# Performance work log

Hardware: AMD Instinct MI355X
Metric: run time of the kernel (lower is better)

## Reference

```python
import jax, jax.numpy as jnp
import numpy as np

B, S, IN = 16, 512, 32
D, H, L = 768, 12, 6
DH = D // H
DFF = 4 * D
EPS = 1e-5
NEG = -1e9


def _ln(x, g, b):
    m = jnp.mean(x, axis=-1, keepdims=True)
    v = jnp.mean(jnp.square(x - m), axis=-1, keepdims=True)
    return (x - m) * jax.lax.rsqrt(v + EPS) * g + b


def setup_inputs() -> dict:
    key = jax.random.key(0)
    ks = jax.random.split(key, 24)
    nrm = lambda k, shape, s=0.02: jax.random.normal(k, shape, jnp.float32) * s
    inp = {
        'x': jax.random.normal(ks[0], (B, S, IN), jnp.float32),
        'event_lengths': jax.random.randint(ks[1], (B,), 1, S + 1),
        'in_w': nrm(ks[2], (IN, D)),
        'in_b': jnp.zeros((D,), jnp.float32),
        'pos_emb': nrm(ks[3], (S, D)),
        'qw': nrm(ks[4], (L, D, D)), 'qb': jnp.zeros((L, D), jnp.float32),
        'kw': nrm(ks[5], (L, D, D)), 'kb': jnp.zeros((L, D), jnp.float32),
        'vw': nrm(ks[6], (L, D, D)), 'vb': jnp.zeros((L, D), jnp.float32),
        'w1': nrm(ks[7], (L, D, DFF)), 'b1': jnp.zeros((L, DFF), jnp.float32),
        'w2': nrm(ks[8], (L, DFF, D)), 'b2': jnp.zeros((L, D), jnp.float32),
        'ln1_g': jnp.ones((L, D), jnp.float32), 'ln1_b': jnp.zeros((L, D), jnp.float32),
        'ln2_g': jnp.ones((L, D), jnp.float32), 'ln2_b': jnp.zeros((L, D), jnp.float32),
        'out_w': nrm(ks[9], (D, 1)), 'out_b': jnp.zeros((1,), jnp.float32),
    }
    return inp


def reference(x, event_lengths, in_w, in_b, pos_emb, qw, qb, kw, kb, vw, vb,
              w1, b1, w2, b2, ln1_g, ln1_b, ln2_g, ln2_b, out_w, out_b):
    b, s, _ = x.shape
    h = x @ in_w + in_b + pos_emb[None, :s]  # [B,S,D]
    valid = jnp.arange(s)[None, :] < event_lengths[:, None]  # [B,S]
    amask = valid[:, None, :, None] & valid[:, None, None, :]  # [B,1,S,S]
    scale = np.float32(1.0 / np.sqrt(DH))
    for l in range(qw.shape[0]):
        q = (h @ qw[l] + qb[l]).reshape(b, s, H, DH)
        k = (h @ kw[l] + kb[l]).reshape(b, s, H, DH)
        v = (h @ vw[l] + vb[l]).reshape(b, s, H, DH)
        scores = jnp.einsum('bqhd,bkhd->bhqk', q, k) * scale
        scores = jnp.where(amask, scores, NEG)
        p = jax.nn.softmax(scores, axis=-1)
        o = jnp.einsum('bhqk,bkhd->bqhd', p, v).reshape(b, s, -1)
        # NOTE: source overwrites summarize(...) output with the raw concat, so no out-proj
        h = _ln(h + o, ln1_g[l], ln1_b[l])
        ff = jnp.maximum(h @ w1[l] + b1[l], 0.0) @ w2[l] + b2[l]
        h = _ln(h + ff, ln2_g[l], ln2_b[l])
    pooled = jnp.where(valid[..., None], h, 0.0).sum(axis=1) / event_lengths[:, None].astype(h.dtype)
    return pooled @ out_w + out_b  # [B,1]
```

## Files before the change

### kernel.cpp

```cpp
#include <hip/hip_runtime.h>

typedef unsigned short u16;
typedef unsigned int u32;
typedef u16 u16x8 __attribute__((ext_vector_type(8)));
typedef u16 u16x4 __attribute__((ext_vector_type(4)));
typedef __bf16 bf16x8 __attribute__((ext_vector_type(8)));
typedef float f32x4 __attribute__((ext_vector_type(4)));

#define DEV __device__ __forceinline__

DEV u16 f2bf(float f) {
  u32 u = __builtin_bit_cast(u32, f);
  u32 r = u + 0x7fffu + ((u >> 16) & 1u);
  return (u16)(r >> 16);
}

DEV float bf2f(u16 v) { return __builtin_bit_cast(float, (u32)v << 16); }

DEV int imin(int a, int b) { return a < b ? a : b; }

DEV void gload_lds16(const void* g, void* l) {
  __builtin_amdgcn_global_load_lds(
      (const __attribute__((address_space(1))) void*)g,
      (__attribute__((address_space(3))) void*)l, 16, 0, 0);
}

template <int RELU, int VMODE>
__global__ __launch_bounds__(256, 3) void gemm97_kernel(
    const u16* __restrict__ A, const u16* __restrict__ Bt, const float* __restrict__ bias,
    u16* __restrict__ Cb, u16* __restrict__ vT, const int* __restrict__ lens, int M, int N, int K,
    int ldc) {
  __shared__ __align__(16) u16 As[128 * 64];
  __shared__ __align__(16) u16 Bs[128 * 64];
  const int t = threadIdx.x, wave = t >> 6, lane = t & 63;
  const int fr = lane & 15, fq = lane >> 4;
  const int NT = K >> 6;
  const int nbx = N >> 7;

  int bid = blockIdx.x;
  {
    const int cpx = (int)gridDim.x >> 3;
    bid = (bid & 7) * cpx + (bid >> 3);
  }
  const int bx = bid % nbx, by = bid / nbx;
  const int m0 = by << 7, n0 = bx << 7;
  if ((m0 & 511) >= lens[m0 >> 9]) return;

  const int srow = t >> 3;
  const int c8 = ((t & 7) ^ (srow & 7)) * 8;
  const u16* ag = A + (size_t)(m0 + srow) * K + c8;
  const u16* bg = Bt + (size_t)(n0 + srow) * K + c8;
  char* asb = (char*)As + wave * 1024;
  char* bsb = (char*)Bs + wave * 1024;

  const int wr = (wave >> 1) * 64, wc = (wave & 1) * 64;
  f32x4 acc[4][4] = {};

  for (int k0 = 0; k0 < NT; ++k0) {
#pragma unroll
    for (int i = 0; i < 4; ++i) {
      gload_lds16(ag + (size_t)i * 32 * K, asb + i * 4096);
      gload_lds16(bg + (size_t)i * 32 * K, bsb + i * 4096);
    }
    ag += 64;
    bg += 64;
    asm volatile("s_waitcnt vmcnt(0)" ::: "memory");
    __syncthreads();
#pragma unroll
    for (int ks = 0; ks < 2; ++ks) {
      bf16x8 af[4], bv[4];
#pragma unroll
      for (int m = 0; m < 4; ++m)
        af[m] = *(const bf16x8*)(As + (wr + m * 16 + fr) * 64 + (((ks * 4 + fq) ^ (fr & 7)) * 8));
#pragma unroll
      for (int n = 0; n < 4; ++n)
        bv[n] = *(const bf16x8*)(Bs + (wc + n * 16 + fr) * 64 + (((ks * 4 + fq) ^ (fr & 7)) * 8));
#pragma unroll
      for (int m = 0; m < 4; ++m)
#pragma unroll
        for (int n = 0; n < 4; ++n)
          acc[m][n] = __builtin_amdgcn_mfma_f32_16x16x32_bf16(af[m], bv[n], acc[m][n], 0, 0, 0);
    }
    __syncthreads();
  }

#pragma unroll
  for (int n = 0; n < 4; ++n) {
    const int colb = n0 + wc + n * 16;
    const int col = colb + fr;
    const float bvv = bias[col];
    if (VMODE && colb >= 1536) {
      const int dd = col - 1536;
      const int hh = dd >> 6, d6 = dd & 63;
#pragma unroll
      for (int m = 0; m < 4; ++m) {
        const int row0 = m0 + wr + m * 16 + fq * 4;
        const int bb = row0 >> 9, ss = row0 & 511;
        u16x4 pk;
#pragma unroll
        for (int r = 0; r < 4; ++r) pk[r] = f2bf(acc[m][n][r] + bvv);
        *(u16x4*)(vT + ((size_t)(bb * 12 + hh) * 64 + d6) * 512 + ss) = pk;
      }
    } else {
#pragma unroll
      for (int m = 0; m < 4; ++m) {
#pragma unroll
        for (int r = 0; r < 4; ++r) {
          const int row = m0 + wr + m * 16 + fq * 4 + r;
          float v = acc[m][n][r] + bvv;
          if (RELU) v = fmaxf(v, 0.f);
          Cb[(size_t)row * ldc + col] = f2bf(v);
        }
      }
    }
  }
}

__global__ __launch_bounds__(256) void attn_kernel(const u16* __restrict__ qk,
                                                   const u16* __restrict__ vT,
                                                   const int* __restrict__ lens,
                                                   u16* __restrict__ o) {
  __shared__ __align__(16) u16 Kl[128 * 64];
  __shared__ __align__(16) u16 Vt[64 * 128];
  __shared__ __align__(16) u16 Pl[4][16 * 128];

  const int bid = blockIdx.x;
  const int z = bid & 1;
  const int pair = bid >> 1;
  const int h = pair % 12;
  const int b = pair / 12;
  const int len = lens[b];
  if (z * 256 >= len) return;
  const int t = threadIdx.x, wave = t >> 6, lane = t & 63;
  const int fr = lane & 15, fq = lane >> 4;

  const size_t base = (size_t)b * 512 * 1536;
  const size_t vbase = (size_t)(b * 12 + h) * 64 * 512;
  const int q0w = z * 256 + wave * 64;

  bf16x8 qf[4][2];
#pragma unroll
  for (int qi = 0; qi < 4; ++qi)
#pragma unroll
    for (int ks = 0; ks < 2; ++ks)
      qf[qi][ks] = *(const bf16x8*)(qk + base + (size_t)(q0w + qi * 16 + fr) * 1536 + h * 64 +
                                    ks * 32 + fq * 8);

  f32x4 oacc[4][4] = {};
  float mrow[4][4], lrow[4][4];
#pragma unroll
  for (int qi = 0; qi < 4; ++qi)
#pragma unroll
    for (int r = 0; r < 4; ++r) {
      mrow[qi][r] = -1e30f;
      lrow[qi][r] = 0.f;
    }

  const int nt = (len + 127) >> 7;
  for (int kt = 0; kt < nt; ++kt) {
    const int kv0 = kt * 128;
#pragma unroll
    for (int i = 0; i < 4; ++i) {
      const int c = i * 256 + t;
      const int krow = c >> 3, kch = c & 7;
      u16x8 kvl = *(const u16x8*)(qk + base + (size_t)(kv0 + krow) * 1536 + 768 + h * 64 + kch * 8);
      *(u16x8*)(Kl + krow * 64 + ((kch ^ (krow & 7)) * 8)) = kvl;
      const int d = c >> 4, vch = c & 15;
      u16x8 vv = *(const u16x8*)(vT + vbase + (size_t)d * 512 + kv0 + vch * 8);
      *(u16x8*)(Vt + d * 128 + ((vch ^ (d & 7)) * 8)) = vv;
    }
    __syncthreads();

#pragma unroll
    for (int qi = 0; qi < 4; ++qi) {
      if (q0w + qi * 16 >= len) break;
      f32x4 sa[8] = {};
#pragma unroll
      for (int ks = 0; ks < 2; ++ks) {
#pragma unroll
        for (int n = 0; n < 8; ++n) {
          const int colr = n * 16 + fr;
          bf16x8 kf = *(const bf16x8*)(Kl + colr * 64 + (((ks * 4 + fq) ^ (colr & 7)) * 8));
          sa[n] = __builtin_amdgcn_mfma_f32_16x16x32_bf16(qf[qi][ks], kf, sa[n], 0, 0, 0);
        }
      }

      float tm[4] = {-1e30f, -1e30f, -1e30f, -1e30f};
#pragma unroll
      for (int n = 0; n < 8; ++n) {
        const int col = kv0 + n * 16 + fr;
        const bool ok = col < len;
#pragma unroll
        for (int r = 0; r < 4; ++r) {
          const float s = ok ? sa[n][r] * 0.125f : -1e30f;
          sa[n][r] = s;
          tm[r] = fmaxf(tm[r], s);
        }
      }
#pragma unroll
      for (int d = 1; d < 16; d <<= 1)
#pragma unroll
        for (int r = 0; r < 4; ++r) tm[r] = fmaxf(tm[r], __shfl_xor(tm[r], d));

      float al[4], rs[4];
#pragma unroll
      for (int r = 0; r < 4; ++r) {
        const float mn = fmaxf(mrow[qi][r], tm[r]);
        al[r] = __expf(mrow[qi][r] - mn);
        mrow[qi][r] = mn;
        rs[r] = 0.f;
      }
#pragma unroll
      for (int n = 0; n < 8; ++n)
#pragma unroll
        for (int r = 0; r < 4; ++r) {
          const float p = __expf(sa[n][r] - mrow[qi][r]);
          sa[n][r] = p;
          rs[r] += p;
        }
#pragma unroll
      for (int d = 1; d < 16; d <<= 1)
#pragma unroll
        for (int r = 0; r < 4; ++r) rs[r] += __shfl_xor(rs[r], d);
#pragma unroll
      for (int r = 0; r < 4; ++r) lrow[qi][r] = lrow[qi][r] * al[r] + rs[r];
#pragma unroll
      for (int n = 0; n < 4; ++n)
#pragma unroll
        for (int r = 0; r < 4; ++r) oacc[qi][n][r] *= al[r];

      u16* P = &Pl[wave][0];
#pragma unroll
      for (int n = 0; n < 8; ++n) {
        const int col = n * 16 + fr;
#pragma unroll
        for (int r = 0; r < 4; ++r) {
          const int row = fq * 4 + r;
          P[row * 128 + (((col >> 3) ^ (row & 7)) * 8) + (col & 7)] = f2bf(sa[n][r]);
        }
      }
#pragma unroll
      for (int kslot = 0; kslot < 4; ++kslot) {
        const int ch = kslot * 4 + fq;
        bf16x8 pa = *(const bf16x8*)(P + fr * 128 + ((ch ^ (fr & 7)) * 8));
#pragma unroll
        for (int n = 0; n < 4; ++n) {
          const int colv = n * 16 + fr;
          bf16x8 vf = *(const bf16x8*)(Vt + colv * 128 + ((ch ^ (colv & 7)) * 8));
          oacc[qi][n] = __builtin_amdgcn_mfma_f32_16x16x32_bf16(pa, vf, oacc[qi][n], 0, 0, 0);
        }
      }
    }
    __syncthreads();
  }

  const size_t obase = (size_t)b * 512 * 768 + (size_t)q0w * 768 + h * 64;
#pragma unroll
  for (int qi = 0; qi < 4; ++qi) {
    if (q0w + qi * 16 >= len) break;
#pragma unroll
    for (int n = 0; n < 4; ++n)
#pragma unroll
      for (int r = 0; r < 4; ++r)
        o[obase + (size_t)(qi * 16 + fq * 4 + r) * 768 + n * 16 + fr] =
            f2bf(oacc[qi][n][r] / lrow[qi][r]);
  }
}

__global__ __launch_bounds__(256) void transpose_all_kernel(
    const float* __restrict__ qw, const float* __restrict__ kw, const float* __restrict__ vw,
    const float* __restrict__ w1, const float* __restrict__ w2, u16* __restrict__ qkvt6,
    u16* __restrict__ w1t6, u16* __restrict__ w2t6) {
  __shared__ float tile[64][65];
  const int l = blockIdx.y;
  int x = blockIdx.x;
  const float* in;
  u16* op;
  int K, N, nbx;
  if (x < 432) {
    const int which = x / 144;
    x -= which * 144;
    in = (which == 0 ? qw : which == 1 ? kw : vw) + (size_t)l * 768 * 768;
    op = qkvt6 + (size_t)l * 2304 * 768 + (size_t)which * 768 * 768;
    K = 768;
    N = 768;
    nbx = 12;
  } else if (x < 1008) {
    x -= 432;
    in = w1 + (size_t)l * 768 * 3072;
    op = w1t6 + (size_t)l * 3072 * 768;
    K = 768;
    N = 3072;
    nbx = 48;
  } else {
    x -= 1008;
    in = w2 + (size_t)l * 3072 * 768;
    op = w2t6 + (size_t)l * 768 * 3072;
    K = 3072;
    N = 768;
    nbx = 12;
  }
  const int tx = threadIdx.x & 63, ty = threadIdx.x >> 6;
  const int n0 = (x % nbx) * 64, k0 = (x / nbx) * 64;
#pragma unroll
  for (int i = 0; i < 16; ++i)
    tile[ty + i * 4][tx] = in[(size_t)(k0 + ty + i * 4) * N + n0 + tx];
  __syncthreads();
#pragma unroll
  for (int i = 0; i < 16; ++i)
    op[(size_t)(n0 + ty + i * 4) * K + k0 + tx] = f2bf(tile[tx][ty + i * 4]);
}

__global__ __launch_bounds__(256) void inproj_kernel(const float* __restrict__ x,
                                                     const float* __restrict__ in_w,
                                                     const float* __restrict__ in_b,
                                                     const float* __restrict__ pos,
                                                     float* __restrict__ h,
                                                     u16* __restrict__ hbf) {
  __shared__ float xs[8][32];
  const int t = threadIdx.x;
  const int row0 = blockIdx.x * 8;
  xs[t >> 5][t & 31] = x[(size_t)row0 * 32 + t];
  __syncthreads();
#pragma unroll
  for (int j = 0; j < 3; ++j) {
    const int d = t + j * 256;
    float acc[8] = {};
#pragma unroll
    for (int i = 0; i < 32; ++i) {
      const float wv = in_w[i * 768 + d];
#pragma unroll
      for (int r = 0; r < 8; ++r) acc[r] += xs[r][i] * wv;
    }
    const float bb = in_b[d];
#pragma unroll
    for (int r = 0; r < 8; ++r) {
      const int row = row0 + r;
      const int s = row & 511;
      const float v = acc[r] + bb + pos[(size_t)s * 768 + d];
      h[(size_t)row * 768 + d] = v;
      hbf[(size_t)row * 768 + d] = f2bf(v);
    }
  }
}

__global__ __launch_bounds__(256) void ln_kernel(const float* __restrict__ hin,
                                                 const u16* __restrict__ delta,
                                                 const int* __restrict__ lens,
                                                 const float* __restrict__ g,
                                                 const float* __restrict__ bb,
                                                 float* __restrict__ hout,
                                                 u16* __restrict__ hbf) {
  const int row = blockIdx.x * 4 + (threadIdx.x >> 6);
  if ((row & 511) >= lens[row >> 9]) return;
  const int lane = threadIdx.x & 63;
  const size_t rb = (size_t)row * 768 + lane * 4;
  f32x4 xv[3];
  float s = 0.f, s2 = 0.f;
#pragma unroll
  for (int j = 0; j < 3; ++j) {
    f32x4 a = *(const f32x4*)(hin + rb + j * 256);
    u16x4 dv = *(const u16x4*)(delta + rb + j * 256);
    f32x4 v;
#pragma unroll
    for (int c = 0; c < 4; ++c) v[c] = a[c] + bf2f(dv[c]);
    xv[j] = v;
    s += v[0] + v[1] + v[2] + v[3];
    s2 += v[0] * v[0] + v[1] * v[1] + v[2] * v[2] + v[3] * v[3];
  }
#pragma unroll
  for (int d = 1; d < 64; d <<= 1) {
    s += __shfl_xor(s, d);
    s2 += __shfl_xor(s2, d);
  }
  const float mean = s * (1.f / 768.f);
  const float var = fmaxf(s2 * (1.f / 768.f) - mean * mean, 0.f);
  const float rstd = rsqrtf(var + 1e-5f);
#pragma unroll
  for (int j = 0; j < 3; ++j) {
    f32x4 gv = *(const f32x4*)(g + lane * 4 + j * 256);
    f32x4 bv = *(const f32x4*)(bb + lane * 4 + j * 256);
    f32x4 y;
    u16x4 yb;
#pragma unroll
    for (int c = 0; c < 4; ++c) {
      y[c] = (xv[j][c] - mean) * rstd * gv[c] + bv[c];
      yb[c] = f2bf(y[c]);
    }
    *(f32x4*)(hout + rb + j * 256) = y;
    *(u16x4*)(hbf + rb + j * 256) = yb;
  }
}

__global__ __launch_bounds__(256) void pool1_kernel(const float* __restrict__ h,
                                                    const int* __restrict__ lens,
                                                    const float* __restrict__ ow,
                                                    float* __restrict__ wsp) {
  const int b = blockIdx.x >> 3, chunk = blockIdx.x & 7;
  const int len = lens[b];
  const int t = threadIdx.x;
  const int s0 = chunk * 64;
  const int s1 = imin(s0 + 64, len);
  float acc0 = 0.f, acc1 = 0.f, acc2 = 0.f;
  const float* hp = h + (size_t)b * 512 * 768;
  for (int s = s0; s < s1; ++s) {
    const size_t rb = (size_t)s * 768;
    acc0 += hp[rb + t];
    acc1 += hp[rb + t + 256];
    acc2 += hp[rb + t + 512];
  }
  float part = acc0 * ow[t] + acc1 * ow[t + 256] + acc2 * ow[t + 512];
#pragma unroll
  for (int d = 1; d < 64; d <<= 1) part += __shfl_xor(part, d);
  __shared__ float ps[4];
  if ((t & 63) == 0) ps[t >> 6] = part;
  __syncthreads();
  if (t == 0) wsp[blockIdx.x] = ps[0] + ps[1] + ps[2] + ps[3];
}

__global__ void pool2_kernel(const float* __restrict__ wsp, const int* __restrict__ lens,
                             const float* __restrict__ ob, float* __restrict__ out) {
  const int b = threadIdx.x;
  if (b < 16) {
    float s = 0.f;
#pragma unroll
    for (int c = 0; c < 8; ++c) s += wsp[b * 8 + c];
    out[b] = s / (float)lens[b] + ob[0];
  }
}

__global__ void biaspack_kernel(const float* __restrict__ qb, const float* __restrict__ kb,
                                const float* __restrict__ vb, float* __restrict__ qkvb) {
  const int i = blockIdx.x * 256 + threadIdx.x;
  if (i >= 6 * 2304) return;
  const int l = i / 2304, j = i % 2304;
  float v;
  if (j < 768)
    v = qb[l * 768 + j];
  else if (j < 1536)
    v = kb[l * 768 + j - 768];
  else
    v = vb[l * 768 + j - 1536];
  qkvb[i] = v;
}

extern "C" void kernel_launch(void* const* d_in, const int* in_sizes, int n_in, void* d_out,
                              int out_size, void* d_ws, size_t ws_size, hipStream_t stream) {
  const float* x = (const float*)d_in[0];
  const int* lens = (const int*)d_in[1];
  const float* in_w = (const float*)d_in[2];
  const float* in_b = (const float*)d_in[3];
  const float* pos = (const float*)d_in[4];
  const float* qw = (const float*)d_in[5];
  const float* qb = (const float*)d_in[6];
  const float* kw = (const float*)d_in[7];
  const float* kb = (const float*)d_in[8];
  const float* vw = (const float*)d_in[9];
  const float* vb = (const float*)d_in[10];
  const float* w1 = (const float*)d_in[11];
  const float* b1 = (const float*)d_in[12];
  const float* w2 = (const float*)d_in[13];
  const float* b2 = (const float*)d_in[14];
  const float* ln1g = (const float*)d_in[15];
  const float* ln1b = (const float*)d_in[16];
  const float* ln2g = (const float*)d_in[17];
  const float* ln2b = (const float*)d_in[18];
  const float* ow = (const float*)d_in[19];
  const float* ob = (const float*)d_in[20];
  float* out = (float*)d_out;

  char* w = (char*)d_ws;
  size_t off = 0;
  auto alloc = [&](size_t bytes) -> void* {
    void* p = w + off;
    off += (bytes + 255) & ~(size_t)255;
    return p;
  };
  u16* qkvt6 = (u16*)alloc((size_t)6 * 2304 * 768 * 2);
  u16* w1t6 = (u16*)alloc((size_t)6 * 3072 * 768 * 2);
  u16* w2t6 = (u16*)alloc((size_t)6 * 768 * 3072 * 2);
  float* qkvb = (float*)alloc((size_t)6 * 2304 * 4);
  float* h = (float*)alloc((size_t)8192 * 768 * 4);
  u16* hbf = (u16*)alloc((size_t)8192 * 768 * 2);
  u16* obuf = (u16*)alloc((size_t)8192 * 768 * 2);
  u16* ubuf = (u16*)alloc((size_t)8192 * 3072 * 2);
  float* wsp = (float*)alloc((size_t)128 * 4);
  u16* qkbuf = ubuf;
  u16* vT = ubuf + (size_t)8192 * 1536;
  u16* ffbuf = ubuf;

  biaspack_kernel<<<(6 * 2304 + 255) / 256, 256, 0, stream>>>(qb, kb, vb, qkvb);
  transpose_all_kernel<<<dim3(1584, 6), 256, 0, stream>>>(qw, kw, vw, w1, w2, qkvt6, w1t6, w2t6);
  inproj_kernel<<<1024, 256, 0, stream>>>(x, in_w, in_b, pos, h, hbf);

  for (int l = 0; l < 6; ++l) {
    gemm97_kernel<0, 1><<<1152, 256, 0, stream>>>(hbf, qkvt6 + (size_t)l * 2304 * 768,
                                                  qkvb + l * 2304, qkbuf, vT, lens, 8192, 2304,
                                                  768, 1536);
    attn_kernel<<<384, 256, 0, stream>>>(qkbuf, vT, lens, obuf);
    ln_kernel<<<2048, 256, 0, stream>>>(h, obuf, lens, ln1g + l * 768, ln1b + l * 768, h, hbf);
    gemm97_kernel<1, 0><<<1536, 256, 0, stream>>>(hbf, w1t6 + (size_t)l * 3072 * 768,
                                                  b1 + l * 3072, ffbuf, nullptr, lens, 8192, 3072,
                                                  768, 3072);
    gemm97_kernel<0, 0><<<384, 256, 0, stream>>>(ffbuf, w2t6 + (size_t)l * 768 * 3072,
                                                 b2 + l * 768, obuf, nullptr, lens, 8192, 768,
                                                 3072, 768);
    ln_kernel<<<2048, 256, 0, stream>>>(h, obuf, lens, ln2g + l * 768, ln2b + l * 768, h, hbf);
  }
  pool1_kernel<<<128, 256, 0, stream>>>(h, lens, ow, wsp);
  pool2_kernel<<<1, 64, 0, stream>>>(wsp, lens, ob, out);
  (void)in_sizes;
  (void)n_in;
  (void)out_size;
  (void)ws_size;
}
```

Measured before the change: 1.383 ms.

## Double-buffer FFN1 GEMM, widen attention to 8 waves, vectorize weight transpose

Adds a PIPE template option to the GEMM that double-buffers the LDS tiles, so the next K-tile's global-to-LDS loads are issued before the current tile's MFMAs. It is enabled only for the FFN up-projection, with occupancy lowered to 2 blocks per CU to fit the doubled shared memory. The attention kernel now runs 512 threads, each wave handling 32 query rows instead of 64, to raise parallelism and cut per-wave register use. The weight transpose kernel now uses vectorized float4 loads, a bf16 LDS tile and packed 4-element stores.

```diff
diff --git a/kernel.cpp b/kernel.cpp
--- a/kernel.cpp
+++ b/kernel.cpp
@@ -25,13 +25,13 @@
       (__attribute__((address_space(3))) void*)l, 16, 0, 0);
 }
 
-template <int RELU, int VMODE>
-__global__ __launch_bounds__(256, 3) void gemm97_kernel(
+template <int RELU, int VMODE, int PIPE>
+__global__ __launch_bounds__(256, PIPE ? 2 : 3) void gemm97_kernel(
     const u16* __restrict__ A, const u16* __restrict__ Bt, const float* __restrict__ bias,
     u16* __restrict__ Cb, u16* __restrict__ vT, const int* __restrict__ lens, int M, int N, int K,
     int ldc) {
-  __shared__ __align__(16) u16 As[128 * 64];
-  __shared__ __align__(16) u16 Bs[128 * 64];
+  __shared__ __align__(16) u16 As[(PIPE ? 2 : 1) * 128 * 64];
+  __shared__ __align__(16) u16 Bs[(PIPE ? 2 : 1) * 128 * 64];
   const int t = threadIdx.x, wave = t >> 6, lane = t & 63;
   const int fr = lane & 15, fq = lane >> 4;
   const int NT = K >> 6;
@@ -50,37 +50,55 @@
   const int c8 = ((t & 7) ^ (srow & 7)) * 8;
   const u16* ag = A + (size_t)(m0 + srow) * K + c8;
   const u16* bg = Bt + (size_t)(n0 + srow) * K + c8;
-  char* asb = (char*)As + wave * 1024;
-  char* bsb = (char*)Bs + wave * 1024;
+
+  auto STAGE = [&](int buf, int kt) {
+    char* a = (char*)As + buf * 16384 + wave * 1024;
+    char* b = (char*)Bs + buf * 16384 + wave * 1024;
+    const u16* agp = ag + (size_t)kt * 64;
+    const u16* bgp = bg + (size_t)kt * 64;
+#pragma unroll
+    for (int i = 0; i < 4; ++i) {
+      gload_lds16(agp + (size_t)i * 32 * K, a + i * 4096);
+      gload_lds16(bgp + (size_t)i * 32 * K, b + i * 4096);
+    }
+  };
 
   const int wr = (wave >> 1) * 64, wc = (wave & 1) * 64;
   f32x4 acc[4][4] = {};
 
-  for (int k0 = 0; k0 < NT; ++k0) {
-#pragma unroll
-    for (int i = 0; i < 4; ++i) {
-      gload_lds16(ag + (size_t)i * 32 * K, asb + i * 4096);
-      gload_lds16(bg + (size_t)i * 32 * K, bsb + i * 4096);
-    }
-    ag += 64;
-    bg += 64;
+  if (PIPE) {
+    STAGE(0, 0);
     asm volatile("s_waitcnt vmcnt(0)" ::: "memory");
     __syncthreads();
+  }
+
+  for (int kt = 0; kt < NT; ++kt) {
+    const int cur = PIPE ? (kt & 1) : 0;
+    if (PIPE) {
+      if (kt + 1 < NT) STAGE(cur ^ 1, kt + 1);
+    } else {
+      STAGE(0, kt);
+      asm volatile("s_waitcnt vmcnt(0)" ::: "memory");
+      __syncthreads();
+    }
+    const u16* Ab = As + cur * 8192;
+    const u16* Bb = Bs + cur * 8192;
 #pragma unroll
     for (int ks = 0; ks < 2; ++ks) {
       bf16x8 af[4], bv[4];
 #pragma unroll
       for (int m = 0; m < 4; ++m)
-        af[m] = *(const bf16x8*)(As + (wr + m * 16 + fr) * 64 + (((ks * 4 + fq) ^ (fr & 7)) * 8));
+        af[m] = *(const bf16x8*)(Ab + (wr + m * 16 + fr) * 64 + (((ks * 4 + fq) ^ (fr & 7)) * 8));
 #pragma unroll
       for (int n = 0; n < 4; ++n)
-        bv[n] = *(const bf16x8*)(Bs + (wc + n * 16 + fr) * 64 + (((ks * 4 + fq) ^ (fr & 7)) * 8));
+        bv[n] = *(const bf16x8*)(Bb + (wc + n * 16 + fr) * 64 + (((ks * 4 + fq) ^ (fr & 7)) * 8));
 #pragma unroll
       for (int m = 0; m < 4; ++m)
 #pragma unroll
         for (int n = 0; n < 4; ++n)
           acc[m][n] = __builtin_amdgcn_mfma_f32_16x16x32_bf16(af[m], bv[n], acc[m][n], 0, 0, 0);
     }
+    if (PIPE) asm volatile("s_waitcnt vmcnt(0)" ::: "memory");
     __syncthreads();
   }
 
@@ -116,13 +134,13 @@
   }
 }
 
-__global__ __launch_bounds__(256) void attn_kernel(const u16* __restrict__ qk,
+__global__ __launch_bounds__(512) void attn_kernel(const u16* __restrict__ qk,
                                                    const u16* __restrict__ vT,
                                                    const int* __restrict__ lens,
                                                    u16* __restrict__ o) {
   __shared__ __align__(16) u16 Kl[128 * 64];
   __shared__ __align__(16) u16 Vt[64 * 128];
-  __shared__ __align__(16) u16 Pl[4][16 * 128];
+  __shared__ __align__(16) u16 Pl[8][16 * 128];
 
   const int bid = blockIdx.x;
   const int z = bid & 1;
@@ -136,20 +154,20 @@
 
   const size_t base = (size_t)b * 512 * 1536;
   const size_t vbase = (size_t)(b * 12 + h) * 64 * 512;
-  const int q0w = z * 256 + wave * 64;
-
-  bf16x8 qf[4][2];
-#pragma unroll
-  for (int qi = 0; qi < 4; ++qi)
+  const int q0w = z * 256 + wave * 32;
+
+  bf16x8 qf[2][2];
+#pragma unroll
+  for (int qi = 0; qi < 2; ++qi)
 #pragma unroll
     for (int ks = 0; ks < 2; ++ks)
       qf[qi][ks] = *(const bf16x8*)(qk + base + (size_t)(q0w + qi * 16 + fr) * 1536 + h * 64 +
                                     ks * 32 + fq * 8);
 
-  f32x4 oacc[4][4] = {};
-  float mrow[4][4], lrow[4][4];
-#pragma unroll
-  for (int qi = 0; qi < 4; ++qi)
+  f32x4 oacc[2][4] = {};
+  float mrow[2][4], lrow[2][4];
+#pragma unroll
+  for (int qi = 0; qi < 2; ++qi)
 #pragma unroll
     for (int r = 0; r < 4; ++r) {
       mrow[qi][r] = -1e30f;
@@ -160,8 +178,8 @@
   for (int kt = 0; kt < nt; ++kt) {
     const int kv0 = kt * 128;
 #pragma unroll
-    for (int i = 0; i < 4; ++i) {
-      const int c = i * 256 + t;
+    for (int i = 0; i < 2; ++i) {
+      const int c = i * 512 + t;
       const int krow = c >> 3, kch = c & 7;
       u16x8 kvl = *(const u16x8*)(qk + base + (size_t)(kv0 + krow) * 1536 + 768 + h * 64 + kch * 8);
       *(u16x8*)(Kl + krow * 64 + ((kch ^ (krow & 7)) * 8)) = kvl;
@@ -172,7 +190,7 @@
     __syncthreads();
 
 #pragma unroll
-    for (int qi = 0; qi < 4; ++qi) {
+    for (int qi = 0; qi < 2; ++qi) {
       if (q0w + qi * 16 >= len) break;
       f32x4 sa[8] = {};
 #pragma unroll
@@ -256,7 +274,7 @@
 
   const size_t obase = (size_t)b * 512 * 768 + (size_t)q0w * 768 + h * 64;
 #pragma unroll
-  for (int qi = 0; qi < 4; ++qi) {
+  for (int qi = 0; qi < 2; ++qi) {
     if (q0w + qi * 16 >= len) break;
 #pragma unroll
     for (int n = 0; n < 4; ++n)
@@ -271,7 +289,7 @@
     const float* __restrict__ qw, const float* __restrict__ kw, const float* __restrict__ vw,
     const float* __restrict__ w1, const float* __restrict__ w2, u16* __restrict__ qkvt6,
     u16* __restrict__ w1t6, u16* __restrict__ w2t6) {
-  __shared__ float tile[64][65];
+  __shared__ u16 tile[64 * 66];
   const int l = blockIdx.y;
   int x = blockIdx.x;
   const float* in;
@@ -300,15 +318,25 @@
     N = 768;
     nbx = 12;
   }
-  const int tx = threadIdx.x & 63, ty = threadIdx.x >> 6;
   const int n0 = (x % nbx) * 64, k0 = (x / nbx) * 64;
-#pragma unroll
-  for (int i = 0; i < 16; ++i)
-    tile[ty + i * 4][tx] = in[(size_t)(k0 + ty + i * 4) * N + n0 + tx];
+  const int lr = threadIdx.x >> 4;
+  const int lc = threadIdx.x & 15;
+#pragma unroll
+  for (int i = 0; i < 4; ++i) {
+    const int kr = i * 16 + lr;
+    f32x4 v = *(const f32x4*)(in + (size_t)(k0 + kr) * N + n0 + lc * 4);
+#pragma unroll
+    for (int j = 0; j < 4; ++j) tile[(lc * 4 + j) * 66 + kr] = f2bf(v[j]);
+  }
   __syncthreads();
 #pragma unroll
-  for (int i = 0; i < 16; ++i)
-    op[(size_t)(n0 + ty + i * 4) * K + k0 + tx] = f2bf(tile[tx][ty + i * 4]);
+  for (int i = 0; i < 4; ++i) {
+    const int nr = i * 16 + lr;
+    u16x4 pk;
+#pragma unroll
+    for (int j = 0; j < 4; ++j) pk[j] = tile[nr * 66 + lc * 4 + j];
+    *(u16x4*)(op + (size_t)(n0 + nr) * K + k0 + lc * 4) = pk;
+  }
 }
 
 __global__ __launch_bounds__(256) void inproj_kernel(const float* __restrict__ x,
@@ -494,17 +522,17 @@
   inproj_kernel<<<1024, 256, 0, stream>>>(x, in_w, in_b, pos, h, hbf);
 
   for (int l = 0; l < 6; ++l) {
-    gemm97_kernel<0, 1><<<1152, 256, 0, stream>>>(hbf, qkvt6 + (size_t)l * 2304 * 768,
-                                                  qkvb + l * 2304, qkbuf, vT, lens, 8192, 2304,
-                                                  768, 1536);
-    attn_kernel<<<384, 256, 0, stream>>>(qkbuf, vT, lens, obuf);
+    gemm97_kernel<0, 1, 0><<<1152, 256, 0, stream>>>(hbf, qkvt6 + (size_t)l * 2304 * 768,
+                                                     qkvb + l * 2304, qkbuf, vT, lens, 8192, 2304,
+                                                     768, 1536);
+    attn_kernel<<<384, 512, 0, stream>>>(qkbuf, vT, lens, obuf);
     ln_kernel<<<2048, 256, 0, stream>>>(h, obuf, lens, ln1g + l * 768, ln1b + l * 768, h, hbf);
-    gemm97_kernel<1, 0><<<1536, 256, 0, stream>>>(hbf, w1t6 + (size_t)l * 3072 * 768,
-                                                  b1 + l * 3072, ffbuf, nullptr, lens, 8192, 3072,
-                                                  768, 3072);
-    gemm97_kernel<0, 0><<<384, 256, 0, stream>>>(ffbuf, w2t6 + (size_t)l * 768 * 3072,
-                                                 b2 + l * 768, obuf, nullptr, lens, 8192, 768,
-                                                 3072, 768);
+    gemm97_kernel<1, 0, 1><<<1536, 256, 0, stream>>>(hbf, w1t6 + (size_t)l * 3072 * 768,
+                                                     b1 + l * 3072, ffbuf, nullptr, lens, 8192,
+                                                     3072, 768, 3072);
+    gemm97_kernel<0, 0, 0><<<384, 256, 0, stream>>>(ffbuf, w2t6 + (size_t)l * 768 * 3072,
+                                                    b2 + l * 768, obuf, nullptr, lens, 8192, 768,
+                                                    3072, 768);
     ln_kernel<<<2048, 256, 0, stream>>>(h, obuf, lens, ln2g + l * 768, ln2b + l * 768, h, hbf);
   }
   pool1_kernel<<<128, 256, 0, stream>>>(h, lens, ow, wsp);
```

Measured after the change: 1.324 ms (median of 2 runs). 4.3% less time.
